# Kernel tuning notes

Measured on AMD Instinct MI355X. Metric: run time of the kernel, lower is better.

Reference implementation:

```python
import jax, jax.numpy as jnp
import numpy as np

DIM = 64
HEADS = 4
HEAD_DIM = DIM // HEADS
HIDDEN = DIM * 2
B, N = 8, 2048


def _layernorm(x, g, b, eps=1e-5):
    mu = jnp.mean(x, axis=-1, keepdims=True)
    var = jnp.var(x, axis=-1, keepdims=True)
    return (x - mu) * jax.lax.rsqrt(var + eps) * g + b


def setup_inputs() -> dict:
    key = jax.random.key(0)
    ks = jax.random.split(key, 12)
    s = 0.02
    return {
        "x": jax.random.normal(ks[0], (B, N, DIM), jnp.float32),
        "clinic": jax.random.normal(ks[1], (B, N, DIM), jnp.float32),
        "norm1_g": jnp.ones((DIM,), jnp.float32),
        "norm1_b": jnp.zeros((DIM,), jnp.float32),
        "norm2_g": jnp.ones((DIM,), jnp.float32),
        "norm2_b": jnp.zeros((DIM,), jnp.float32),
        "Wkv": jax.random.normal(ks[2], (DIM, 2 * DIM), jnp.float32) * s,
        "bkv": jnp.zeros((2 * DIM,), jnp.float32),
        "Wq": jax.random.normal(ks[3], (DIM, DIM), jnp.float32) * s,
        "bq": jnp.zeros((DIM,), jnp.float32),
        "Wproj": jax.random.normal(ks[4], (DIM, DIM), jnp.float32) * s,
        "bproj": jnp.zeros((DIM,), jnp.float32),
        "W1": jax.random.normal(ks[5], (DIM, HIDDEN), jnp.float32) * s,
        "b1": jnp.zeros((HIDDEN,), jnp.float32),
        "W2": jax.random.normal(ks[6], (HIDDEN, DIM), jnp.float32) * s,
        "b2": jnp.zeros((DIM,), jnp.float32),
    }


def reference(x, clinic, norm1_g, norm1_b, norm2_g, norm2_b,
              Wkv, bkv, Wq, bq, Wproj, bproj, W1, b1, W2, b2):
    # shared norm1 on both streams (as in the torch code)
    xn = _layernorm(x, norm1_g, norm1_b)
    cn = _layernorm(clinic, norm1_g, norm1_b)
    scale = HEAD_DIM ** -0.5
    # K/V from x, Q from clinic
    kv = (xn @ Wkv + bkv).reshape(B, N, 2, HEADS, HEAD_DIM)
    k = kv[:, :, 0].transpose(0, 2, 1, 3)  # [B,H,N,hd]
    v = kv[:, :, 1].transpose(0, 2, 1, 3)
    q = (cn @ Wq + bq).reshape(B, N, HEADS, HEAD_DIM).transpose(0, 2, 1, 3)
    attn = jax.nn.softmax(jnp.einsum('bhqd,bhkd->bhqk', q, k) * scale, axis=-1)
    o = jnp.einsum('bhqk,bhkd->bhqd', attn, v).transpose(0, 2, 1, 3).reshape(B, N, DIM)
    o = o @ Wproj + bproj
    # MLP with residual (dropout/drop_path are inference no-ops)
    h = _layernorm(o, norm2_g, norm2_b)
    h = jax.nn.gelu(h @ W1 + b1, approximate=False) @ W2 + b2
    return o + h
```

## Files before the change

kernel.cpp:

```cpp
#include <hip/hip_runtime.h>
#include <hip/hip_bf16.h>
#include <math.h>

#define B_    8
#define N_    2048
#define DIM_  64
#define H_    4
#define HD_   16
#define HID_  128
#define NROWS (B_ * N_)
#define KVB   64
#define QSCALE (0.25f * 1.4426950408889634f)

typedef float    f32x4 __attribute__((ext_vector_type(4)));
typedef __fp16   hfx2  __attribute__((ext_vector_type(2)));
typedef _Float16 f16x4 __attribute__((ext_vector_type(4)));
typedef _Float16 f16x8 __attribute__((ext_vector_type(8)));

#define MFMA16(a, b, c) __builtin_amdgcn_mfma_f32_16x16x16f16((a), (b), (c), 0, 0, 0)

__device__ __forceinline__ float ex2(float x) {
#if __has_builtin(__builtin_amdgcn_exp2f)
    return __builtin_amdgcn_exp2f(x);
#else
    return exp2f(x);
#endif
}

__global__ __launch_bounds__(256) void k1_ln_qkv(
    const float* __restrict__ x, const float* __restrict__ clinic,
    const float* __restrict__ n1g, const float* __restrict__ n1b,
    const float* __restrict__ Wkv, const float* __restrict__ bkv,
    const float* __restrict__ Wq,  const float* __restrict__ bq,
    _Float16* __restrict__ Kd, _Float16* __restrict__ Vd,
    _Float16* __restrict__ Qd)
{
    __shared__ _Float16 WkvT[128][68];
    __shared__ _Float16 WqT [64][68];
    __shared__ _Float16 xnT [64][68];
    __shared__ _Float16 cnT [64][68];

    const int tid  = threadIdx.x;
    const int row0 = blockIdx.x * 64;

    for (int i = tid; i < 64 * 128; i += 256) {
        const int d = i >> 7, c = i & 127;
        WkvT[c][d] = (_Float16)Wkv[i];
    }
    for (int i = tid; i < 64 * 64; i += 256) {
        const int d = i >> 6, c = i & 63;
        WqT[c][d] = (_Float16)Wq[i];
    }

    {
        const int r = tid >> 4, s = tid & 15;
        const float4 gv = *(const float4*)(n1g + s * 4);
        const float4 bv = *(const float4*)(n1b + s * 4);
        #pragma unroll
        for (int it = 0; it < 4; ++it) {
            const int rl = it * 16 + r;
            const int rg = row0 + rl;
            float4 xv = *(const float4*)(x      + (size_t)rg * DIM_ + s * 4);
            float4 cv = *(const float4*)(clinic + (size_t)rg * DIM_ + s * 4);

            float xs = xv.x + xv.y + xv.z + xv.w;
            float cs = cv.x + cv.y + cv.z + cv.w;
            #pragma unroll
            for (int m = 1; m < 16; m <<= 1) {
                xs += __shfl_xor(xs, m);
                cs += __shfl_xor(cs, m);
            }
            const float xmu = xs * (1.f / 64.f);
            const float cmu = cs * (1.f / 64.f);
            float4 xd = make_float4(xv.x - xmu, xv.y - xmu, xv.z - xmu, xv.w - xmu);
            float4 cd = make_float4(cv.x - cmu, cv.y - cmu, cv.z - cmu, cv.w - cmu);

            float xq = xd.x * xd.x + xd.y * xd.y + xd.z * xd.z + xd.w * xd.w;
            float cq = cd.x * cd.x + cd.y * cd.y + cd.z * cd.z + cd.w * cd.w;
            #pragma unroll
            for (int m = 1; m < 16; m <<= 1) {
                xq += __shfl_xor(xq, m);
                cq += __shfl_xor(cq, m);
            }
            const float xinv = rsqrtf(xq * (1.f / 64.f) + 1e-5f);
            const float cinv = rsqrtf(cq * (1.f / 64.f) + 1e-5f);

            xnT[rl][s * 4 + 0] = (_Float16)(xd.x * xinv * gv.x + bv.x);
            xnT[rl][s * 4 + 1] = (_Float16)(xd.y * xinv * gv.y + bv.y);
            xnT[rl][s * 4 + 2] = (_Float16)(xd.z * xinv * gv.z + bv.z);
            xnT[rl][s * 4 + 3] = (_Float16)(xd.w * xinv * gv.w + bv.w);
            cnT[rl][s * 4 + 0] = (_Float16)(cd.x * cinv * gv.x + bv.x);
            cnT[rl][s * 4 + 1] = (_Float16)(cd.y * cinv * gv.y + bv.y);
            cnT[rl][s * 4 + 2] = (_Float16)(cd.z * cinv * gv.z + bv.z);
            cnT[rl][s * 4 + 3] = (_Float16)(cd.w * cinv * gv.w + bv.w);
        }
    }
    __syncthreads();

    const int lane = tid & 63, wave = tid >> 6;
    const int col  = lane & 15;
    const int grp4 = (lane >> 4) * 4;
    const int arow = wave * 16 + col;
    const f32x4 Z = {0.f, 0.f, 0.f, 0.f};

    f16x4 ax[4], ac[4];
    #pragma unroll
    for (int kt = 0; kt < 4; ++kt) {
        ax[kt] = *(const f16x4*)&xnT[arow][kt * 16 + grp4];
        ac[kt] = *(const f16x4*)&cnT[arow][kt * 16 + grp4];
    }

    #pragma unroll
    for (int ct = 0; ct < 8; ++ct) {
        f32x4 acc = Z;
        #pragma unroll
        for (int kt = 0; kt < 4; ++kt) {
            const f16x4 bf = *(const f16x4*)&WkvT[ct * 16 + col][kt * 16 + grp4];
            acc = MFMA16(ax[kt], bf, acc);
        }
        const int c = ct * 16 + col;
        const float bias = bkv[c];
        _Float16* dst = (c & 64) ? Vd : Kd;
        const int hh = (c >> 4) & 3, dd = c & 15;
        #pragma unroll
        for (int r = 0; r < 4; ++r) {
            const int rg = row0 + wave * 16 + grp4 + r;
            const int b = rg >> 11, n = rg & (N_ - 1);
            dst[(((size_t)(b * H_ + hh)) * N_ + n) * HD_ + dd] =
                (_Float16)(acc[r] + bias);
        }
    }
    #pragma unroll
    for (int ct = 0; ct < 4; ++ct) {
        f32x4 acc = Z;
        #pragma unroll
        for (int kt = 0; kt < 4; ++kt) {
            const f16x4 bf = *(const f16x4*)&WqT[ct * 16 + col][kt * 16 + grp4];
            acc = MFMA16(ac[kt], bf, acc);
        }
        const int c = ct * 16 + col;
        const float bias = bq[c];
        const int hh = c >> 4, dd = c & 15;
        #pragma unroll
        for (int r = 0; r < 4; ++r) {
            const int rg = row0 + wave * 16 + grp4 + r;
            const int b = rg >> 11, n = rg & (N_ - 1);
            Qd[(((size_t)(b * H_ + hh)) * N_ + n) * HD_ + dd] =
                (_Float16)((acc[r] + bias) * QSCALE);
        }
    }
}

__global__ __launch_bounds__(256, 3) void k2_attn(
    const _Float16* __restrict__ Kd, const _Float16* __restrict__ Vd,
    const _Float16* __restrict__ Qd, float* __restrict__ O)
{
    __shared__ union {
        _Float16 vt[4][2][16][70];
        float    mg[4][64][18];
    } sm;
    __shared__ float smL[4][64];

    const int tid  = threadIdx.x;
    const int lane = tid & 63;
    const int wave = tid >> 6;
    const int col  = lane & 15;
    const int grp4 = (lane >> 4) * 4;

    const int wg = (blockIdx.x & 7) * 128 + (blockIdx.x >> 3);
    const int bh = wg >> 5;
    const int qt = wg & 31;

    const _Float16* Kbh = Kd + (size_t)bh * (N_ * HD_);
    const _Float16* Vbh = Vd + (size_t)bh * (N_ * HD_);
    const _Float16* Qbh = Qd + (size_t)bh * (N_ * HD_);

    const int qbase = qt * 64;
    f16x4 qf[4];
    #pragma unroll
    for (int qp = 0; qp < 4; ++qp)
        qf[qp] = *(const f16x4*)(Qbh + (qbase + qp * 16 + col) * HD_ + grp4);

    const int k0   = wave * 512;
    const int koff = (k0 + col) * HD_ + grp4;
    const int voff = (k0 + lane) * HD_;

    float l0 = 0.f, l1 = 0.f, l2 = 0.f, l3 = 0.f;
    f32x4 o0 = {0.f, 0.f, 0.f, 0.f}, o1 = o0, o2 = o0, o3 = o0;

    f16x4 kf[4];
    #pragma unroll
    for (int sb = 0; sb < 4; ++sb)
        kf[sb] = *(const f16x4*)(Kbh + koff + sb * (16 * HD_));
    {
        const f16x8 va = *(const f16x8*)(Vbh + voff);
        const f16x8 vb = *(const f16x8*)(Vbh + voff + 8);
        #pragma unroll
        for (int hh = 0; hh < 8; ++hh) {
            sm.vt[wave][0][hh][lane]     = va[hh];
            sm.vt[wave][0][hh + 8][lane] = vb[hh];
        }
    }

    int cur = 0;
    for (int kt = 0; kt < 8; ++kt) {
        const int nxo = ((kt + 1) & 7) * (KVB * HD_);
        f16x4 kn[4];
        #pragma unroll
        for (int sb = 0; sb < 4; ++sb)
            kn[sb] = *(const f16x4*)(Kbh + koff + nxo + sb * (16 * HD_));
        const f16x8 vna = *(const f16x8*)(Vbh + voff + nxo);
        const f16x8 vnb = *(const f16x8*)(Vbh + voff + nxo + 8);

        f16x4 vf[4];
        #pragma unroll
        for (int sb = 0; sb < 4; ++sb)
            vf[sb] = *(const f16x4*)&sm.vt[wave][cur][col][sb * 16 + grp4];

        const f32x4 Z = {0.f, 0.f, 0.f, 0.f};
        #pragma unroll
        for (int qp = 0; qp < 4; ++qp) {
            f32x4 s[4];
            #pragma unroll
            for (int sb = 0; sb < 4; ++sb)
                s[sb] = MFMA16(kf[sb], qf[qp], Z);

            float pl = 0.f;
            f16x4 pf[4];
            #pragma unroll
            for (int sb = 0; sb < 4; ++sb) {
                const float a0 = ex2(s[sb][0]), a1 = ex2(s[sb][1]);
                const float a2 = ex2(s[sb][2]), a3 = ex2(s[sb][3]);
                pl += (a0 + a1) + (a2 + a3);
                const hfx2 lo = __builtin_amdgcn_cvt_pkrtz(a0, a1);
                const hfx2 hi = __builtin_amdgcn_cvt_pkrtz(a2, a3);
                pf[sb] = (f16x4){(_Float16)lo[0], (_Float16)lo[1],
                                 (_Float16)hi[0], (_Float16)hi[1]};
            }
            if (qp == 0) { l0 += pl; }
            else if (qp == 1) { l1 += pl; }
            else if (qp == 2) { l2 += pl; }
            else { l3 += pl; }

            f32x4& o = (qp == 0) ? o0 : (qp == 1) ? o1 : (qp == 2) ? o2 : o3;
            #pragma unroll
            for (int sb = 0; sb < 4; ++sb)
                o = MFMA16(pf[sb], vf[sb], o);
        }

        #pragma unroll
        for (int hh = 0; hh < 8; ++hh) {
            sm.vt[wave][cur ^ 1][hh][lane]     = vna[hh];
            sm.vt[wave][cur ^ 1][hh + 8][lane] = vnb[hh];
        }
        kf[0] = kn[0]; kf[1] = kn[1]; kf[2] = kn[2]; kf[3] = kn[3];
        cur ^= 1;
    }

    l0 += __shfl_xor(l0, 16); l0 += __shfl_xor(l0, 32);
    l1 += __shfl_xor(l1, 16); l1 += __shfl_xor(l1, 32);
    l2 += __shfl_xor(l2, 16); l2 += __shfl_xor(l2, 32);
    l3 += __shfl_xor(l3, 16); l3 += __shfl_xor(l3, 32);

    __syncthreads();
    #pragma unroll
    for (int r = 0; r < 4; ++r) {
        sm.mg[wave][ 0 + grp4 + r][col] = o0[r];
        sm.mg[wave][16 + grp4 + r][col] = o1[r];
        sm.mg[wave][32 + grp4 + r][col] = o2[r];
        sm.mg[wave][48 + grp4 + r][col] = o3[r];
    }
    if ((lane >> 4) == 0) {
        smL[wave][ 0 + col] = l0;
        smL[wave][16 + col] = l1;
        smL[wave][32 + col] = l2;
        smL[wave][48 + col] = l3;
    }
    __syncthreads();

    {
        const int q = tid >> 2, h4 = (tid & 3) * 4;
        const float ls = smL[0][q] + smL[1][q] + smL[2][q] + smL[3][q];
        const float rl = 1.f / ls;
        float v[4];
        #pragma unroll
        for (int j = 0; j < 4; ++j)
            v[j] = (sm.mg[0][q][h4 + j] + sm.mg[1][q][h4 + j] +
                    sm.mg[2][q][h4 + j] + sm.mg[3][q][h4 + j]) * rl;
        const int b = bh >> 2, h = bh & 3;
        float* dst = O + ((size_t)b * N_ + qbase + q) * DIM_ + h * HD_ + h4;
        *(float4*)dst = make_float4(v[0], v[1], v[2], v[3]);
    }
}

__device__ __forceinline__ float gelu_fast(float v) {
    const float t = v * v;
    const float z = v * fmaf(0.035677408f, t, 0.79788456f);
    const float e = ex2(z * 2.8853900817779268f);
    const float r = __builtin_amdgcn_rcpf(e + 1.0f);
    return v * e * r;
}

__global__ __launch_bounds__(256) void k3_proj_mlp(
    const float* __restrict__ O,
    const float* __restrict__ Wproj, const float* __restrict__ bproj,
    const float* __restrict__ n2g,   const float* __restrict__ n2b,
    const float* __restrict__ W1,    const float* __restrict__ b1,
    const float* __restrict__ W2,    const float* __restrict__ b2,
    float* __restrict__ out)
{
    __shared__ _Float16 WpT [64][68];
    __shared__ _Float16 W1T [128][68];
    __shared__ _Float16 W2T [64][136];
    __shared__ _Float16 aT  [64][68];
    __shared__ float    sp  [64][68];
    __shared__ _Float16 hT  [64][68];
    __shared__ _Float16 actT[64][136];

    const int tid  = threadIdx.x;
    const int row0 = blockIdx.x * 64;

    for (int i = tid; i < 64 * 64; i += 256) {
        const int k = i >> 6, c = i & 63;
        WpT[c][k] = (_Float16)Wproj[i];
    }
    for (int i = tid; i < 64 * 128; i += 256) {
        const int k = i >> 7, c = i & 127;
        W1T[c][k] = (_Float16)W1[i];
    }
    for (int i = tid; i < 128 * 64; i += 256) {
        const int k = i >> 6, c = i & 63;
        W2T[c][k] = (_Float16)W2[i];
    }
    {
        const int r = tid >> 2, c0 = (tid & 3) * 16;
        const float4* src = (const float4*)(O + (size_t)(row0 + r) * DIM_ + c0);
        #pragma unroll
        for (int j = 0; j < 4; ++j) {
            const float4 v = src[j];
            aT[r][c0 + j * 4 + 0] = (_Float16)v.x;
            aT[r][c0 + j * 4 + 1] = (_Float16)v.y;
            aT[r][c0 + j * 4 + 2] = (_Float16)v.z;
            aT[r][c0 + j * 4 + 3] = (_Float16)v.w;
        }
    }
    __syncthreads();

    const int lane = tid & 63, wave = tid >> 6;
    const int col  = lane & 15;
    const int grp4 = (lane >> 4) * 4;
    const int arow = wave * 16 + col;
    const f32x4 Z = {0.f, 0.f, 0.f, 0.f};

    {
        f16x4 af[4];
        #pragma unroll
        for (int kt = 0; kt < 4; ++kt)
            af[kt] = *(const f16x4*)&aT[arow][kt * 16 + grp4];
        #pragma unroll
        for (int ct = 0; ct < 4; ++ct) {
            f32x4 acc = Z;
            #pragma unroll
            for (int kt = 0; kt < 4; ++kt) {
                const f16x4 bf = *(const f16x4*)&WpT[ct * 16 + col][kt * 16 + grp4];
                acc = MFMA16(af[kt], bf, acc);
            }
            const int c = ct * 16 + col;
            const float bias = bproj[c];
            #pragma unroll
            for (int r = 0; r < 4; ++r)
                sp[wave * 16 + grp4 + r][c] = acc[r] + bias;
        }
    }
    __syncthreads();

    {
        const int r = tid >> 4, s = tid & 15;
        const float4 gv = *(const float4*)(n2g + s * 4);
        const float4 bv = *(const float4*)(n2b + s * 4);
        #pragma unroll
        for (int it = 0; it < 4; ++it) {
            const int rl = it * 16 + r;
            const float4 v = *(const float4*)&sp[rl][s * 4];
            float sm = v.x + v.y + v.z + v.w;
            #pragma unroll
            for (int m = 1; m < 16; m <<= 1) sm += __shfl_xor(sm, m);
            const float mu = sm * (1.f / 64.f);
            float4 d4 = make_float4(v.x - mu, v.y - mu, v.z - mu, v.w - mu);
            float qs = d4.x * d4.x + d4.y * d4.y + d4.z * d4.z + d4.w * d4.w;
            #pragma unroll
            for (int m = 1; m < 16; m <<= 1) qs += __shfl_xor(qs, m);
            const float inv = rsqrtf(qs * (1.f / 64.f) + 1e-5f);
            hT[rl][s * 4 + 0] = (_Float16)(d4.x * inv * gv.x + bv.x);
            hT[rl][s * 4 + 1] = (_Float16)(d4.y * inv * gv.y + bv.y);
            hT[rl][s * 4 + 2] = (_Float16)(d4.z * inv * gv.z + bv.z);
            hT[rl][s * 4 + 3] = (_Float16)(d4.w * inv * gv.w + bv.w);
        }
    }
    __syncthreads();

    {
        f16x4 hf[4];
        #pragma unroll
        for (int kt = 0; kt < 4; ++kt)
            hf[kt] = *(const f16x4*)&hT[arow][kt * 16 + grp4];
        #pragma unroll
        for (int ct = 0; ct < 8; ++ct) {
            f32x4 acc = Z;
            #pragma unroll
            for (int kt = 0; kt < 4; ++kt) {
                const f16x4 bf = *(const f16x4*)&W1T[ct * 16 + col][kt * 16 + grp4];
                acc = MFMA16(hf[kt], bf, acc);
            }
            const int c = ct * 16 + col;
            const float bias = b1[c];
            #pragma unroll
            for (int r = 0; r < 4; ++r)
                actT[wave * 16 + grp4 + r][c] =
                    (_Float16)gelu_fast(acc[r] + bias);
        }
    }

    {
        f16x4 pf[8];
        #pragma unroll
        for (int kt = 0; kt < 8; ++kt)
            pf[kt] = *(const f16x4*)&actT[arow][kt * 16 + grp4];
        #pragma unroll
        for (int ct = 0; ct < 4; ++ct) {
            f32x4 acc = Z;
            #pragma unroll
            for (int kt = 0; kt < 8; ++kt) {
                const f16x4 bf = *(const f16x4*)&W2T[ct * 16 + col][kt * 16 + grp4];
                acc = MFMA16(pf[kt], bf, acc);
            }
            const int c = ct * 16 + col;
            const float bias = b2[c];
            #pragma unroll
            for (int r = 0; r < 4; ++r) {
                const int rl = wave * 16 + grp4 + r;
                out[(size_t)(row0 + rl) * DIM_ + c] = acc[r] + bias + sp[rl][c];
            }
        }
    }
}

extern "C" void kernel_launch(void* const* d_in, const int* in_sizes, int n_in,
                              void* d_out, int out_size, void* d_ws, size_t ws_size,
                              hipStream_t stream) {
    const float* x      = (const float*)d_in[0];
    const float* clinic = (const float*)d_in[1];
    const float* n1g    = (const float*)d_in[2];
    const float* n1b    = (const float*)d_in[3];
    const float* n2g    = (const float*)d_in[4];
    const float* n2b    = (const float*)d_in[5];
    const float* Wkv    = (const float*)d_in[6];
    const float* bkv    = (const float*)d_in[7];
    const float* Wq     = (const float*)d_in[8];
    const float* bq     = (const float*)d_in[9];
    const float* Wproj  = (const float*)d_in[10];
    const float* bproj  = (const float*)d_in[11];
    const float* W1     = (const float*)d_in[12];
    const float* b1     = (const float*)d_in[13];
    const float* W2     = (const float*)d_in[14];
    const float* b2     = (const float*)d_in[15];
    float* out = (float*)d_out;

    char* ws = (char*)d_ws;
    const size_t SZ = (size_t)B_ * H_ * N_ * HD_;
    _Float16* Kd = (_Float16*)ws;
    _Float16* Vd = (_Float16*)(ws + 2 * SZ);
    _Float16* Qd = (_Float16*)(ws + 4 * SZ);
    float*    O  = (float*)   (ws + 6 * SZ);

    k1_ln_qkv<<<NROWS / 64, 256, 0, stream>>>(x, clinic, n1g, n1b, Wkv, bkv,
                                              Wq, bq, Kd, Vd, Qd);
    k2_attn<<<32 * 32, 256, 0, stream>>>(Kd, Vd, Qd, O);
    k3_proj_mlp<<<NROWS / 64, 256, 0, stream>>>(O, Wproj, bproj, n2g, n2b,
                                                W1, b1, W2, b2, out);
}
```

Before: 42.94 us.

## Store V transposed in projection kernel and load MFMA V fragments directly

The QKV kernel now writes V in a per-head transposed [dim][token] layout using packed 4-element stores. This lets the attention kernel load V MFMA fragments straight from global memory instead of staging and transposing through double-buffered shared memory. The per-tile LDS writes and reads are removed, along with one barrier. Launch bounds are raised to allow 4 blocks per SM. The cost is narrower strided 8-byte global loads for V and possible register pressure under the tighter occupancy bound.

```diff
diff --git a/kernel.cpp b/kernel.cpp
--- a/kernel.cpp
+++ b/kernel.cpp
@@ -32,7 +32,7 @@
     const float* __restrict__ n1g, const float* __restrict__ n1b,
     const float* __restrict__ Wkv, const float* __restrict__ bkv,
     const float* __restrict__ Wq,  const float* __restrict__ bq,
-    _Float16* __restrict__ Kd, _Float16* __restrict__ Vd,
+    _Float16* __restrict__ Kd, _Float16* __restrict__ VTd,
     _Float16* __restrict__ Qd)
 {
     __shared__ _Float16 WkvT[128][68];
@@ -110,6 +110,10 @@
         ac[kt] = *(const f16x4*)&cnT[arow][kt * 16 + grp4];
     }
 
+    const int rg0 = row0 + wave * 16 + grp4;
+    const int b   = rg0 >> 11;
+    const int n0  = rg0 & (N_ - 1);
+
     #pragma unroll
     for (int ct = 0; ct < 8; ++ct) {
         f32x4 acc = Z;
@@ -120,14 +124,17 @@
         }
         const int c = ct * 16 + col;
         const float bias = bkv[c];
-        _Float16* dst = (c & 64) ? Vd : Kd;
         const int hh = (c >> 4) & 3, dd = c & 15;
-        #pragma unroll
-        for (int r = 0; r < 4; ++r) {
-            const int rg = row0 + wave * 16 + grp4 + r;
-            const int b = rg >> 11, n = rg & (N_ - 1);
-            dst[(((size_t)(b * H_ + hh)) * N_ + n) * HD_ + dd] =
-                (_Float16)(acc[r] + bias);
+        if (c & 64) {
+            f16x4 v4;
+            #pragma unroll
+            for (int r = 0; r < 4; ++r) v4[r] = (_Float16)(acc[r] + bias);
+            *(f16x4*)(VTd + (((size_t)(b * H_ + hh)) * HD_ + dd) * N_ + n0) = v4;
+        } else {
+            #pragma unroll
+            for (int r = 0; r < 4; ++r)
+                Kd[(((size_t)(b * H_ + hh)) * N_ + n0 + r) * HD_ + dd] =
+                    (_Float16)(acc[r] + bias);
         }
     }
     #pragma unroll
@@ -142,23 +149,17 @@
         const float bias = bq[c];
         const int hh = c >> 4, dd = c & 15;
         #pragma unroll
-        for (int r = 0; r < 4; ++r) {
-            const int rg = row0 + wave * 16 + grp4 + r;
-            const int b = rg >> 11, n = rg & (N_ - 1);
-            Qd[(((size_t)(b * H_ + hh)) * N_ + n) * HD_ + dd] =
+        for (int r = 0; r < 4; ++r)
+            Qd[(((size_t)(b * H_ + hh)) * N_ + n0 + r) * HD_ + dd] =
                 (_Float16)((acc[r] + bias) * QSCALE);
-        }
-    }
-}
-
-__global__ __launch_bounds__(256, 3) void k2_attn(
-    const _Float16* __restrict__ Kd, const _Float16* __restrict__ Vd,
+    }
+}
+
+__global__ __launch_bounds__(256, 4) void k2_attn(
+    const _Float16* __restrict__ Kd, const _Float16* __restrict__ VTd,
     const _Float16* __restrict__ Qd, float* __restrict__ O)
 {
-    __shared__ union {
-        _Float16 vt[4][2][16][70];
-        float    mg[4][64][18];
-    } sm;
+    __shared__ float smO[4][64][18];
     __shared__ float smL[4][64];
 
     const int tid  = threadIdx.x;
@@ -171,9 +172,9 @@
     const int bh = wg >> 5;
     const int qt = wg & 31;
 
-    const _Float16* Kbh = Kd + (size_t)bh * (N_ * HD_);
-    const _Float16* Vbh = Vd + (size_t)bh * (N_ * HD_);
-    const _Float16* Qbh = Qd + (size_t)bh * (N_ * HD_);
+    const _Float16* Kbh = Kd  + (size_t)bh * (N_ * HD_);
+    const _Float16* Vbh = VTd + (size_t)bh * (HD_ * N_);
+    const _Float16* Qbh = Qd  + (size_t)bh * (N_ * HD_);
 
     const int qbase = qt * 64;
     f16x4 qf[4];
@@ -183,39 +184,26 @@
 
     const int k0   = wave * 512;
     const int koff = (k0 + col) * HD_ + grp4;
-    const int voff = (k0 + lane) * HD_;
+    const int voff = col * N_ + k0 + grp4;
 
     float l0 = 0.f, l1 = 0.f, l2 = 0.f, l3 = 0.f;
     f32x4 o0 = {0.f, 0.f, 0.f, 0.f}, o1 = o0, o2 = o0, o3 = o0;
 
-    f16x4 kf[4];
-    #pragma unroll
-    for (int sb = 0; sb < 4; ++sb)
+    f16x4 kf[4], vf[4];
+    #pragma unroll
+    for (int sb = 0; sb < 4; ++sb) {
         kf[sb] = *(const f16x4*)(Kbh + koff + sb * (16 * HD_));
-    {
-        const f16x8 va = *(const f16x8*)(Vbh + voff);
-        const f16x8 vb = *(const f16x8*)(Vbh + voff + 8);
-        #pragma unroll
-        for (int hh = 0; hh < 8; ++hh) {
-            sm.vt[wave][0][hh][lane]     = va[hh];
-            sm.vt[wave][0][hh + 8][lane] = vb[hh];
-        }
-    }
-
-    int cur = 0;
+        vf[sb] = *(const f16x4*)(Vbh + voff + sb * 16);
+    }
+
     for (int kt = 0; kt < 8; ++kt) {
-        const int nxo = ((kt + 1) & 7) * (KVB * HD_);
-        f16x4 kn[4];
-        #pragma unroll
-        for (int sb = 0; sb < 4; ++sb)
-            kn[sb] = *(const f16x4*)(Kbh + koff + nxo + sb * (16 * HD_));
-        const f16x8 vna = *(const f16x8*)(Vbh + voff + nxo);
-        const f16x8 vnb = *(const f16x8*)(Vbh + voff + nxo + 8);
-
-        f16x4 vf[4];
-        #pragma unroll
-        for (int sb = 0; sb < 4; ++sb)
-            vf[sb] = *(const f16x4*)&sm.vt[wave][cur][col][sb * 16 + grp4];
+        const int nx = (kt + 1) & 7;
+        f16x4 kn[4], vn[4];
+        #pragma unroll
+        for (int sb = 0; sb < 4; ++sb) {
+            kn[sb] = *(const f16x4*)(Kbh + koff + nx * (KVB * HD_) + sb * (16 * HD_));
+            vn[sb] = *(const f16x4*)(Vbh + voff + nx * KVB + sb * 16);
+        }
 
         const f32x4 Z = {0.f, 0.f, 0.f, 0.f};
         #pragma unroll
@@ -249,12 +237,7 @@
         }
 
         #pragma unroll
-        for (int hh = 0; hh < 8; ++hh) {
-            sm.vt[wave][cur ^ 1][hh][lane]     = vna[hh];
-            sm.vt[wave][cur ^ 1][hh + 8][lane] = vnb[hh];
-        }
-        kf[0] = kn[0]; kf[1] = kn[1]; kf[2] = kn[2]; kf[3] = kn[3];
-        cur ^= 1;
+        for (int sb = 0; sb < 4; ++sb) { kf[sb] = kn[sb]; vf[sb] = vn[sb]; }
     }
 
     l0 += __shfl_xor(l0, 16); l0 += __shfl_xor(l0, 32);
@@ -262,13 +245,12 @@
     l2 += __shfl_xor(l2, 16); l2 += __shfl_xor(l2, 32);
     l3 += __shfl_xor(l3, 16); l3 += __shfl_xor(l3, 32);
 
-    __syncthreads();
     #pragma unroll
     for (int r = 0; r < 4; ++r) {
-        sm.mg[wave][ 0 + grp4 + r][col] = o0[r];
-        sm.mg[wave][16 + grp4 + r][col] = o1[r];
-        sm.mg[wave][32 + grp4 + r][col] = o2[r];
-        sm.mg[wave][48 + grp4 + r][col] = o3[r];
+        smO[wave][ 0 + grp4 + r][col] = o0[r];
+        smO[wave][16 + grp4 + r][col] = o1[r];
+        smO[wave][32 + grp4 + r][col] = o2[r];
+        smO[wave][48 + grp4 + r][col] = o3[r];
     }
     if ((lane >> 4) == 0) {
         smL[wave][ 0 + col] = l0;
@@ -285,8 +267,8 @@
         float v[4];
         #pragma unroll
         for (int j = 0; j < 4; ++j)
-            v[j] = (sm.mg[0][q][h4 + j] + sm.mg[1][q][h4 + j] +
-                    sm.mg[2][q][h4 + j] + sm.mg[3][q][h4 + j]) * rl;
+            v[j] = (smO[0][q][h4 + j] + smO[1][q][h4 + j] +
+                    smO[2][q][h4 + j] + smO[3][q][h4 + j]) * rl;
         const int b = bh >> 2, h = bh & 3;
         float* dst = O + ((size_t)b * N_ + qbase + q) * DIM_ + h * HD_ + h4;
         *(float4*)dst = make_float4(v[0], v[1], v[2], v[3]);
@@ -468,14 +450,14 @@
 
     char* ws = (char*)d_ws;
     const size_t SZ = (size_t)B_ * H_ * N_ * HD_;
-    _Float16* Kd = (_Float16*)ws;
-    _Float16* Vd = (_Float16*)(ws + 2 * SZ);
-    _Float16* Qd = (_Float16*)(ws + 4 * SZ);
-    float*    O  = (float*)   (ws + 6 * SZ);
+    _Float16* Kd  = (_Float16*)ws;
+    _Float16* VTd = (_Float16*)(ws + 2 * SZ);
+    _Float16* Qd  = (_Float16*)(ws + 4 * SZ);
+    float*    O   = (float*)   (ws + 6 * SZ);
 
     k1_ln_qkv<<<NROWS / 64, 256, 0, stream>>>(x, clinic, n1g, n1b, Wkv, bkv,
-                                              Wq, bq, Kd, Vd, Qd);
-    k2_attn<<<32 * 32, 256, 0, stream>>>(Kd, Vd, Qd, O);
+                                              Wq, bq, Kd, VTd, Qd);
+    k2_attn<<<32 * 32, 256, 0, stream>>>(Kd, VTd, Qd, O);
     k3_proj_mlp<<<NROWS / 64, 256, 0, stream>>>(O, Wproj, bproj, n2g, n2b,
                                                 W1, b1, W2, b2, out);
 }
```

After: 44.18 us. +2.9%, slower.
